# Performance work log

Hardware: AMD Instinct MI355X
Metric: run time of the kernel (lower is better)

Reference implementation:

```python
import jax, jax.numpy as jnp
import numpy as np

N = 100000
E = 1200000
D = 64  # g_dim == h2_dim, heads=1


def setup_inputs() -> dict:
    key = jax.random.key(0)
    ks = jax.random.split(key, 12)
    s = 1.0 / np.sqrt(D)
    node_features = jax.random.normal(ks[0], (N, D), dtype=jnp.float32)
    edge_index = jax.random.randint(ks[1], (2, E), 0, N, dtype=jnp.int64)
    edge_type = jax.random.randint(ks[2], (E,), 0, 4, dtype=jnp.int64)
    Wq = jax.random.uniform(ks[3], (D, D), jnp.float32, -s, s)
    bq = jax.random.uniform(ks[4], (D,), jnp.float32, -s, s)
    Wk = jax.random.uniform(ks[5], (D, D), jnp.float32, -s, s)
    bk = jax.random.uniform(ks[6], (D,), jnp.float32, -s, s)
    Wv = jax.random.uniform(ks[7], (D, D), jnp.float32, -s, s)
    bv = jax.random.uniform(ks[8], (D,), jnp.float32, -s, s)
    Wskip = jax.random.uniform(ks[9], (D, D), jnp.float32, -s, s)
    bskip = jax.random.uniform(ks[10], (D,), jnp.float32, -s, s)
    return dict(node_features=node_features, edge_index=edge_index,
                edge_type=edge_type, Wq=Wq, bq=bq, Wk=Wk, bk=bk,
                Wv=Wv, bv=bv, Wskip=Wskip, bskip=bskip)


def _transformer_conv(x, edge_index, Wq, bq, Wk, bk, Wv, bv, Wskip, bskip):
    src, dst = edge_index[0], edge_index[1]
    q = x @ Wq + bq          # [N, D] queries (for targets)
    k = x @ Wk + bk          # [N, D] keys (for sources)
    v = x @ Wv + bv          # [N, D] values (for sources)
    scale = 1.0 / jnp.sqrt(jnp.asarray(D, x.dtype))
    # per-edge attention logits: (q_dst . k_src) / sqrt(D)   [E]
    logits = jnp.sum(q[dst] * k[src], axis=-1) * scale
    # segment softmax over incoming edges of each destination node
    seg_max = jax.ops.segment_max(logits, dst, num_segments=N)
    seg_max = jnp.where(jnp.isfinite(seg_max), seg_max, 0.0)
    ex = jnp.exp(logits - seg_max[dst])
    seg_sum = jax.ops.segment_sum(ex, dst, num_segments=N)
    alpha = ex / (seg_sum[dst] + 1e-16)                      # [E]
    # attention-weighted scatter-aggregate of source values
    out = jax.ops.segment_sum(alpha[:, None] * v[src], dst, num_segments=N)
    # root/skip connection
    return out + x @ Wskip + bskip


def reference(node_features, edge_index, edge_type, Wq, bq, Wk, bk, Wv, bv, Wskip, bskip):
    # edge_type is accepted but unused, matching the original forward.
    return _transformer_conv(node_features, edge_index, Wq, bq, Wk, bk, Wv, bv, Wskip, bskip)
```

## Files before the change

kernel.cpp:

```cpp
#include <hip/hip_runtime.h>
#include <hip/hip_fp16.h>

#define D 64
#define BSH 9
#define SPLIT_CH 1024
#define NH 512
#define QSCALE 0.18033688f

typedef _Float16 f16x2 __attribute__((ext_vector_type(2)));
typedef _Float16 f16x8 __attribute__((ext_vector_type(8)));
typedef float f32x4 __attribute__((ext_vector_type(4)));

__device__ __forceinline__ float fdot2f(f16x2 a, f16x2 b, float c) {
#if __has_builtin(__builtin_amdgcn_fdot2)
    return __builtin_amdgcn_fdot2(a, b, c, false);
#else
    return fmaf((float)a.x, (float)b.x, fmaf((float)a.y, (float)b.y, c));
#endif
}

__device__ __forceinline__ f16x2 shxor_h2(f16x2 v, int m) {
    int i = __builtin_bit_cast(int, v);
    i = __shfl_xor(i, m);
    return __builtin_bit_cast(f16x2, i);
}

__device__ __forceinline__ unsigned packh2(float a, float b) {
    __half2 h = __floats2half2_rn(a, b);
    return __builtin_bit_cast(unsigned, h);
}

__global__ __launch_bounds__(256) void k_prep(
    const float* __restrict__ Wq, const float* __restrict__ Wk,
    const float* __restrict__ Wv, const float* __restrict__ Wsk,
    const float* __restrict__ bq, const float* __restrict__ bk,
    const float* __restrict__ bv, const float* __restrict__ bsk,
    const int* __restrict__ ei, unsigned* __restrict__ wpk,
    float* __restrict__ ball, int* __restrict__ ghist, int e_cnt)
{
    const int t = threadIdx.x;
    if (blockIdx.x < 32) {
        const int u    = blockIdx.x * 256 + t;
        const int i2   = u & 3;
        const int lane = (u >> 2) & 63;
        const int ks   = (u >> 8) & 1;
        const int mt   = u >> 9;
        const int ncol = mt * 16 + (lane & 15);
        const int k0   = ks * 32 + ((lane >> 4) << 3) + (i2 << 1);
        const float* W; int c; float sc = 1.f;
        if      (ncol <  64) { W = Wq;  c = ncol;       sc = QSCALE; }
        else if (ncol < 128) { W = Wk;  c = ncol - 64;  }
        else if (ncol < 192) { W = Wv;  c = ncol - 128; }
        else                 { W = Wsk; c = ncol - 192; }
        wpk[u] = packh2(W[k0 * 64 + c] * sc, W[(k0 + 1) * 64 + c] * sc);
    } else if (blockIdx.x == 32) {
        float b;
        if      (t <  64) b = bq[t] * QSCALE;
        else if (t < 128) b = bk[t - 64];
        else if (t < 192) b = bv[t - 128];
        else              b = bsk[t - 192];
        ball[t] = b;
    } else {
        __shared__ int h[256];
        h[t] = 0;
        __syncthreads();
        const int hb    = blockIdx.x - 33;
        const int chunk = (e_cnt + NH - 1) / NH;
        const int c0    = hb * chunk;
        const int c1    = min(c0 + chunk, e_cnt);
        for (int i = c0 + t; i < c1; i += 256)
            atomicAdd(&h[ei[e_cnt + i] >> BSH], 1);
        __syncthreads();
        if (h[t]) atomicAdd(&ghist[t], h[t]);
    }
}

__global__ __launch_bounds__(256) void k_splitlin(
    const float* __restrict__ x, const unsigned* __restrict__ wpk,
    const float* __restrict__ ball, const int* __restrict__ ei,
    const int* __restrict__ ghist, int* __restrict__ gcur0,
    unsigned* __restrict__ qh, unsigned* __restrict__ kvh,
    float* __restrict__ out, unsigned* __restrict__ epack,
    int n, int e_cnt, int NSPLIT)
{
    __shared__ __align__(16) union {
        struct {
            unsigned vals[SPLIT_CH];
            unsigned char bkt[SPLIT_CH];
            int hist[256], start[256], cur[256], base[256], s2[256], sg[256];
        } sp;
        _Float16 xsh[16][72];
    } sm;
    const int t = threadIdx.x;

    if (blockIdx.x < NSPLIT) {
        unsigned* vals = sm.sp.vals;
        unsigned char* bkt = sm.sp.bkt;
        int* hist  = sm.sp.hist;
        int* start = sm.sp.start;
        int* cur   = sm.sp.cur;
        int* base  = sm.sp.base;
        int* s2    = sm.sp.s2;
        int* sg    = sm.sp.sg;

        const int e0  = blockIdx.x * SPLIT_CH;
        const int cnt = min(SPLIT_CH, e_cnt - e0);

        hist[t] = 0;
        __syncthreads();
        for (int i = t; i < cnt; i += 256)
            atomicAdd(&hist[ei[e_cnt + e0 + i] >> BSH], 1);
        __syncthreads();

        {
            const int v = hist[t];
            const int g = ghist[t];
            s2[t] = v;
            sg[t] = g;
            __syncthreads();
            for (int off = 1; off < 256; off <<= 1) {
                const int a1 = (t >= off) ? s2[t - off] : 0;
                const int a2 = (t >= off) ? sg[t - off] : 0;
                __syncthreads();
                s2[t] += a1;
                sg[t] += a2;
                __syncthreads();
            }
            start[t] = s2[t] - v;
            cur[t]   = s2[t] - v;
            base[t]  = v ? (sg[t] - g + atomicAdd(&gcur0[t], v)) : 0;
        }
        __syncthreads();

        for (int i = t; i < cnt; i += 256) {
            const int s = ei[e0 + i];
            const int d = ei[e_cnt + e0 + i];
            const int b = d >> BSH;
            const int r = atomicAdd(&cur[b], 1);
            vals[r] = ((unsigned)s << BSH) | (unsigned)(d & 511);
            bkt[r]  = (unsigned char)b;
        }
        __syncthreads();

        for (int i = t; i < cnt; i += 256) {
            const int b = bkt[i];
            epack[base[b] + (i - start[b])] = vals[i];
        }
        return;
    }

    const int node0 = (blockIdx.x - NSPLIT) * 16;
    {
        const float4* xg = (const float4*)(x + (size_t)node0 * 64);
        const int row = t >> 4, c4 = (t & 15) << 2;
        if (node0 + row < n) {
            const float4 v = xg[t];
            f16x2* dst = (f16x2*)&sm.xsh[row][c4];
            dst[0] = f16x2{(_Float16)v.x, (_Float16)v.y};
            dst[1] = f16x2{(_Float16)v.z, (_Float16)v.w};
        }
    }
    __syncthreads();

    const int w  = t >> 6;
    const int l  = t & 63;
    const int nd = l & 15;
    const int kg = l >> 4;

    f32x4 acc0 = {0.f, 0.f, 0.f, 0.f};
    f32x4 acc1 = acc0, acc2 = acc0, acc3 = acc0;
    const uint4* wpk4 = (const uint4*)wpk;

#pragma unroll
    for (int ks = 0; ks < 2; ++ks) {
        const f16x8 bfrag = *(const f16x8*)&sm.xsh[nd][ks * 32 + kg * 8];
        const int fb = (w * 4 * 2 + ks) * 64 + l;
        const f16x8 a0 = __builtin_bit_cast(f16x8, wpk4[fb]);
        const f16x8 a1 = __builtin_bit_cast(f16x8, wpk4[fb + 128]);
        const f16x8 a2 = __builtin_bit_cast(f16x8, wpk4[fb + 256]);
        const f16x8 a3 = __builtin_bit_cast(f16x8, wpk4[fb + 384]);
        acc0 = __builtin_amdgcn_mfma_f32_16x16x32_f16(a0, bfrag, acc0, 0, 0, 0);
        acc1 = __builtin_amdgcn_mfma_f32_16x16x32_f16(a1, bfrag, acc1, 0, 0, 0);
        acc2 = __builtin_amdgcn_mfma_f32_16x16x32_f16(a2, bfrag, acc2, 0, 0, 0);
        acc3 = __builtin_amdgcn_mfma_f32_16x16x32_f16(a3, bfrag, acc3, 0, 0, 0);
    }

    const int node = node0 + nd;
    if (node >= n) return;

    f32x4 accs[4] = {acc0, acc1, acc2, acc3};
#pragma unroll
    for (int m4 = 0; m4 < 4; ++m4) {
        const int gc = (w * 4 + m4) * 16 + kg * 4;
        const float4 bb = ((const float4*)ball)[gc >> 2];
        const float v0 = accs[m4][0] + bb.x;
        const float v1 = accs[m4][1] + bb.y;
        const float v2 = accs[m4][2] + bb.z;
        const float v3 = accs[m4][3] + bb.w;
        if (w == 3) {
            ((float4*)out)[(size_t)node * 16 + ((gc - 192) >> 2)] =
                make_float4(v0, v1, v2, v3);
        } else {
            uint2 u;
            u.x = packh2(v0, v1);
            u.y = packh2(v2, v3);
            if (w == 0)
                ((uint2*)qh)[(size_t)node * 16 + (gc >> 2)] = u;
            else if (w == 1)
                ((uint2*)kvh)[(size_t)node * 32 + ((gc - 64) >> 2)] = u;
            else
                ((uint2*)kvh)[(size_t)node * 32 + 16 + ((gc - 128) >> 2)] = u;
        }
    }
}

__global__ __launch_bounds__(512) void k_nodesort(
    const unsigned* __restrict__ epack, const int* __restrict__ ghist,
    int* __restrict__ esrc, int* __restrict__ endoff, int n)
{
    __shared__ int h[512], cur[512], s[512];
    __shared__ int sbase;
    const int b = blockIdx.x;
    const int t = threadIdx.x;

    s[t] = (t < 256) ? ghist[t] : 0;
    __syncthreads();
    for (int off = 1; off < 512; off <<= 1) {
        const int add = (t >= off) ? s[t - off] : 0;
        __syncthreads();
        s[t] += add;
        __syncthreads();
    }
    if (t == 0) sbase = (b == 0) ? 0 : s[b - 1];
    __syncthreads();
    const int base = sbase;
    const int cnt  = ghist[b];

    h[t] = 0;
    __syncthreads();
    for (int i = t; i < cnt; i += 512)
        atomicAdd(&h[epack[base + i] & 511], 1);
    __syncthreads();

    const int v = h[t];
    s[t] = v;
    __syncthreads();
    for (int off = 1; off < 512; off <<= 1) {
        const int add = (t >= off) ? s[t - off] : 0;
        __syncthreads();
        s[t] += add;
        __syncthreads();
    }
    cur[t] = s[t] - v;
    const int node = (b << BSH) + t;
    if (node < n) endoff[node] = base + s[t];
    __syncthreads();

    for (int i = t; i < cnt; i += 512) {
        const unsigned p = epack[base + i];
        const int r = atomicAdd(&cur[p & 511], 1);
        esrc[base + r] = (int)(p >> BSH);
    }
}

__global__ __launch_bounds__(256) void k_attn(
    const uint4* __restrict__ qh4, const uint4* __restrict__ kv4,
    const int* __restrict__ endoff, const int* __restrict__ esrc,
    float* __restrict__ out, int n)
{
    const int t = threadIdx.x;
    const int node = blockIdx.x * 4 + (t >> 6);
    if (node >= n) return;
    const int lane = t & 63;
    const int g = lane >> 3;
    const int l = lane & 7;

    const int beg = (node == 0) ? 0 : endoff[node - 1];
    const int end = endoff[node];
    const int last = end - 1;

    float4 o0 = make_float4(0.f, 0.f, 0.f, 0.f);
    float4 o1 = o0;
    if (g == 0) {
        o0 = ((const float4*)out)[(size_t)node * 16 + 2 * l];
        o1 = ((const float4*)out)[(size_t)node * 16 + 2 * l + 1];
    }

    const uint4 qu = qh4[(size_t)node * 8 + l];
    const f16x2* qp = (const f16x2*)&qu;

    f16x2 a0 = {(_Float16)0.f, (_Float16)0.f};
    f16x2 a1 = a0, a2 = a0, a3 = a0;
    float den = 0.f;

    int b2 = beg;
    for (; end - b2 > 8; b2 += 16) {
        const int iA = b2 + 2 * g;
        const int iB = iA + 1;
        const int sA = esrc[min(iA, last)];
        const int sB = esrc[min(iB, last)];
        const uint4 kuA = kv4[(size_t)sA * 16 + l];
        const uint4 vuA = kv4[(size_t)sA * 16 + 8 + l];
        const uint4 kuB = kv4[(size_t)sB * 16 + l];
        const uint4 vuB = kv4[(size_t)sB * 16 + 8 + l];
        const f16x2* kpA = (const f16x2*)&kuA;
        const f16x2* vpA = (const f16x2*)&vuA;
        const f16x2* kpB = (const f16x2*)&kuB;
        const f16x2* vpB = (const f16x2*)&vuB;

        float dA = fdot2f(qp[0], kpA[0], 0.f);
        float dB = fdot2f(qp[0], kpB[0], 0.f);
        dA = fdot2f(qp[1], kpA[1], dA);
        dB = fdot2f(qp[1], kpB[1], dB);
        dA = fdot2f(qp[2], kpA[2], dA);
        dB = fdot2f(qp[2], kpB[2], dB);
        dA = fdot2f(qp[3], kpA[3], dA);
        dB = fdot2f(qp[3], kpB[3], dB);
        dA += __shfl_xor(dA, 1);  dB += __shfl_xor(dB, 1);
        dA += __shfl_xor(dA, 2);  dB += __shfl_xor(dB, 2);
        dA += __shfl_xor(dA, 4);  dB += __shfl_xor(dB, 4);

        const float eA = (iA < end) ? exp2f(dA) : 0.f;
        const float eB = (iB < end) ? exp2f(dB) : 0.f;
        den += eA + eB;
        const _Float16 ehA = (_Float16)eA;
        const _Float16 ehB = (_Float16)eB;
        const f16x2 e2A = {ehA, ehA};
        const f16x2 e2B = {ehB, ehB};
        a0 += e2A * vpA[0];  a0 += e2B * vpB[0];
        a1 += e2A * vpA[1];  a1 += e2B * vpB[1];
        a2 += e2A * vpA[2];  a2 += e2B * vpB[2];
        a3 += e2A * vpA[3];  a3 += e2B * vpB[3];
    }
    for (; b2 < end; b2 += 8) {
        const int i = b2 + g;
        const int s = esrc[min(i, last)];
        const uint4 ku = kv4[(size_t)s * 16 + l];
        const uint4 vu = kv4[(size_t)s * 16 + 8 + l];
        const f16x2* kp = (const f16x2*)&ku;
        const f16x2* vp = (const f16x2*)&vu;

        float d = fdot2f(qp[0], kp[0], 0.f);
        d = fdot2f(qp[1], kp[1], d);
        d = fdot2f(qp[2], kp[2], d);
        d = fdot2f(qp[3], kp[3], d);
        d += __shfl_xor(d, 1);
        d += __shfl_xor(d, 2);
        d += __shfl_xor(d, 4);

        const float e = (i < end) ? exp2f(d) : 0.f;
        den += e;
        const _Float16 eh = (_Float16)e;
        const f16x2 e2 = {eh, eh};
        a0 += e2 * vp[0];
        a1 += e2 * vp[1];
        a2 += e2 * vp[2];
        a3 += e2 * vp[3];
    }

#pragma unroll
    for (int m = 8; m <= 32; m <<= 1) {
        den += __shfl_xor(den, m);
        a0 += shxor_h2(a0, m);
        a1 += shxor_h2(a1, m);
        a2 += shxor_h2(a2, m);
        a3 += shxor_h2(a3, m);
    }

    if (g == 0) {
        const float inv = 1.f / (den + 1e-16f);
        float4 r0, r1;
        r0.x = o0.x + (float)a0.x * inv;
        r0.y = o0.y + (float)a0.y * inv;
        r0.z = o0.z + (float)a1.x * inv;
        r0.w = o0.w + (float)a1.y * inv;
        r1.x = o1.x + (float)a2.x * inv;
        r1.y = o1.y + (float)a2.y * inv;
        r1.z = o1.z + (float)a3.x * inv;
        r1.w = o1.w + (float)a3.y * inv;
        ((float4*)out)[(size_t)node * 16 + 2 * l]     = r0;
        ((float4*)out)[(size_t)node * 16 + 2 * l + 1] = r1;
    }
}

extern "C" void kernel_launch(void* const* d_in, const int* in_sizes, int n_in,
                              void* d_out, int out_size, void* d_ws, size_t ws_size,
                              hipStream_t stream)
{
    const float* x   = (const float*)d_in[0];
    const int*   ei  = (const int*)d_in[1];
    const float* Wq  = (const float*)d_in[3];
    const float* bq  = (const float*)d_in[4];
    const float* Wk  = (const float*)d_in[5];
    const float* bk  = (const float*)d_in[6];
    const float* Wv  = (const float*)d_in[7];
    const float* bv  = (const float*)d_in[8];
    const float* Wsk = (const float*)d_in[9];
    const float* bsk = (const float*)d_in[10];
    float* out = (float*)d_out;

    const int n      = in_sizes[0] / D;
    const int e_cnt  = in_sizes[1] / 2;
    const int nbkt   = (n + 511) >> BSH;
    const int NLIN   = (n + 15) / 16;
    const int NSPLIT = (e_cnt + SPLIT_CH - 1) / SPLIT_CH;

    unsigned* qh     = (unsigned*)d_ws;
    unsigned* kvh    = qh + (size_t)n * 32;
    int*      esrc   = (int*)(kvh + (size_t)n * 64);
    unsigned* epack  = (unsigned*)(esrc + e_cnt);
    int*      endoff = (int*)(epack + e_cnt);
    int*      ghist  = endoff + n;
    int*      gcur0  = ghist + 256;
    float*    ball   = (float*)(gcur0 + 256);
    unsigned* wpk    = (unsigned*)(ball + 256);

    hipMemsetAsync(ghist, 0, 512 * sizeof(int), stream);

    k_prep<<<33 + NH, 256, 0, stream>>>(
        Wq, Wk, Wv, Wsk, bq, bk, bv, bsk, ei, wpk, ball, ghist, e_cnt);

    k_splitlin<<<NSPLIT + NLIN, 256, 0, stream>>>(
        x, wpk, ball, ei, ghist, gcur0, qh, kvh, out, epack, n, e_cnt, NSPLIT);

    k_nodesort<<<nbkt, 512, 0, stream>>>(
        epack, ghist, esrc, endoff, n);

    k_attn<<<(n + 3) / 4, 256, 0, stream>>>(
        (const uint4*)qh, (const uint4*)kvh, endoff, esrc, out, n);
}
```

Before: 134.6 us.

## Fuse all stages into one cooperative persistent kernel with grid syncs

Replaces the four separate launches (prep/histogram, split+linear, node sort, attention) with a single cooperative kernel that uses grid-wide syncs between phases and grid-stride loops over work. The aim is to remove launch gaps and tail effects between kernels. The split chunk size is doubled, and the node-sort phase now runs with 256 threads handling two nodes each. In exchange it adds grid barriers, depends on cooperative launch and occupancy queries on the host, and caps the persistent grid size, which may reduce parallelism in the attention phase.

```diff
diff --git a/kernel.cpp b/kernel.cpp
--- a/kernel.cpp
+++ b/kernel.cpp
@@ -1,10 +1,12 @@
 #include <hip/hip_runtime.h>
 #include <hip/hip_fp16.h>
+#include <hip/hip_cooperative_groups.h>
+
+namespace cg = cooperative_groups;
 
 #define D 64
 #define BSH 9
-#define SPLIT_CH 1024
-#define NH 512
+#define SPLIT_CH 2048
 #define QSCALE 0.18033688f
 
 typedef _Float16 f16x2 __attribute__((ext_vector_type(2)));
@@ -30,17 +32,42 @@
     return __builtin_bit_cast(unsigned, h);
 }
 
-__global__ __launch_bounds__(256) void k_prep(
-    const float* __restrict__ Wq, const float* __restrict__ Wk,
-    const float* __restrict__ Wv, const float* __restrict__ Wsk,
-    const float* __restrict__ bq, const float* __restrict__ bk,
-    const float* __restrict__ bv, const float* __restrict__ bsk,
-    const int* __restrict__ ei, unsigned* __restrict__ wpk,
-    float* __restrict__ ball, int* __restrict__ ghist, int e_cnt)
+union SMem {
+    int hist0[256];
+    struct {
+        unsigned vals[SPLIT_CH];
+        unsigned char bkt[SPLIT_CH];
+        int hist[256], start[256], cur[256], base[256], s2[256], sg[256];
+    } sp;
+    struct { __align__(16) _Float16 xsh[16][72]; } lin;
+    struct { int h[512], ex[512], cur[512], sA[256]; } ns;
+};
+
+__global__ __launch_bounds__(256, 8) void k_mega(
+    const float* __restrict__ x, const int* __restrict__ ei,
+    const float* __restrict__ Wq, const float* __restrict__ bq,
+    const float* __restrict__ Wk, const float* __restrict__ bk,
+    const float* __restrict__ Wv, const float* __restrict__ bv,
+    const float* __restrict__ Wsk, const float* __restrict__ bsk,
+    unsigned* __restrict__ wpk, float* __restrict__ ball,
+    int* __restrict__ ghist, int* __restrict__ gcur0,
+    unsigned* __restrict__ qh, unsigned* __restrict__ kvh,
+    unsigned* __restrict__ epack, int* __restrict__ esrc,
+    int* __restrict__ endoff, float* __restrict__ out,
+    int n, int e_cnt)
 {
-    const int t = threadIdx.x;
-    if (blockIdx.x < 32) {
-        const int u    = blockIdx.x * 256 + t;
+    __shared__ SMem sm;
+    cg::grid_group gg = cg::this_grid();
+    const int nb  = (int)gridDim.x;
+    const int bid = (int)blockIdx.x;
+    const int t   = (int)threadIdx.x;
+
+    const int NLIN   = (n + 15) >> 4;
+    const int NSPLIT = (e_cnt + SPLIT_CH - 1) / SPLIT_CH;
+    const int nbkt   = (n + 511) >> BSH;
+
+    if (bid < 32) {
+        const int u    = bid * 256 + t;
         const int i2   = u & 3;
         const int lane = (u >> 2) & 63;
         const int ks   = (u >> 8) & 1;
@@ -53,333 +80,311 @@
         else if (ncol < 192) { W = Wv;  c = ncol - 128; }
         else                 { W = Wsk; c = ncol - 192; }
         wpk[u] = packh2(W[k0 * 64 + c] * sc, W[(k0 + 1) * 64 + c] * sc);
-    } else if (blockIdx.x == 32) {
+    } else if (bid == 32) {
         float b;
         if      (t <  64) b = bq[t] * QSCALE;
         else if (t < 128) b = bk[t - 64];
         else if (t < 192) b = bv[t - 128];
         else              b = bsk[t - 192];
         ball[t] = b;
-    } else {
-        __shared__ int h[256];
+    }
+    {
+        int* h = sm.hist0;
         h[t] = 0;
         __syncthreads();
-        const int hb    = blockIdx.x - 33;
-        const int chunk = (e_cnt + NH - 1) / NH;
-        const int c0    = hb * chunk;
-        const int c1    = min(c0 + chunk, e_cnt);
-        for (int i = c0 + t; i < c1; i += 256)
+        for (int i = bid * 256 + t; i < e_cnt; i += nb * 256)
             atomicAdd(&h[ei[e_cnt + i] >> BSH], 1);
         __syncthreads();
         if (h[t]) atomicAdd(&ghist[t], h[t]);
     }
-}
-
-__global__ __launch_bounds__(256) void k_splitlin(
-    const float* __restrict__ x, const unsigned* __restrict__ wpk,
-    const float* __restrict__ ball, const int* __restrict__ ei,
-    const int* __restrict__ ghist, int* __restrict__ gcur0,
-    unsigned* __restrict__ qh, unsigned* __restrict__ kvh,
-    float* __restrict__ out, unsigned* __restrict__ epack,
-    int n, int e_cnt, int NSPLIT)
-{
-    __shared__ __align__(16) union {
-        struct {
-            unsigned vals[SPLIT_CH];
-            unsigned char bkt[SPLIT_CH];
-            int hist[256], start[256], cur[256], base[256], s2[256], sg[256];
-        } sp;
-        _Float16 xsh[16][72];
-    } sm;
-    const int t = threadIdx.x;
-
-    if (blockIdx.x < NSPLIT) {
-        unsigned* vals = sm.sp.vals;
-        unsigned char* bkt = sm.sp.bkt;
-        int* hist  = sm.sp.hist;
-        int* start = sm.sp.start;
-        int* cur   = sm.sp.cur;
-        int* base  = sm.sp.base;
-        int* s2    = sm.sp.s2;
-        int* sg    = sm.sp.sg;
-
-        const int e0  = blockIdx.x * SPLIT_CH;
-        const int cnt = min(SPLIT_CH, e_cnt - e0);
-
-        hist[t] = 0;
+    gg.sync();
+
+    const int SP = min(NSPLIT, nb >> 1);
+    if (bid < SP) {
+        for (int cidx = bid; cidx < NSPLIT; cidx += SP) {
+            const int e0  = cidx * SPLIT_CH;
+            const int cnt = min(SPLIT_CH, e_cnt - e0);
+
+            sm.sp.hist[t] = 0;
+            __syncthreads();
+            for (int i = t; i < cnt; i += 256)
+                atomicAdd(&sm.sp.hist[ei[e_cnt + e0 + i] >> BSH], 1);
+            __syncthreads();
+
+            {
+                const int v = sm.sp.hist[t];
+                const int g = ghist[t];
+                sm.sp.s2[t] = v;
+                sm.sp.sg[t] = g;
+                __syncthreads();
+                for (int off = 1; off < 256; off <<= 1) {
+                    const int a1 = (t >= off) ? sm.sp.s2[t - off] : 0;
+                    const int a2 = (t >= off) ? sm.sp.sg[t - off] : 0;
+                    __syncthreads();
+                    sm.sp.s2[t] += a1;
+                    sm.sp.sg[t] += a2;
+                    __syncthreads();
+                }
+                sm.sp.start[t] = sm.sp.s2[t] - v;
+                sm.sp.cur[t]   = sm.sp.s2[t] - v;
+                sm.sp.base[t]  = v ? (sm.sp.sg[t] - g + atomicAdd(&gcur0[t], v)) : 0;
+            }
+            __syncthreads();
+
+            for (int i = t; i < cnt; i += 256) {
+                const int s = ei[e0 + i];
+                const int d = ei[e_cnt + e0 + i];
+                const int b = d >> BSH;
+                const int r = atomicAdd(&sm.sp.cur[b], 1);
+                sm.sp.vals[r] = ((unsigned)s << BSH) | (unsigned)(d & 511);
+                sm.sp.bkt[r]  = (unsigned char)b;
+            }
+            __syncthreads();
+
+            for (int i = t; i < cnt; i += 256) {
+                const int b = sm.sp.bkt[i];
+                epack[sm.sp.base[b] + (i - sm.sp.start[b])] = sm.sp.vals[i];
+            }
+            __syncthreads();
+        }
+    } else {
+        const int lb  = bid - SP;
+        const int nlb = nb - SP;
+        const uint4* wpk4 = (const uint4*)wpk;
+        for (int tile = lb; tile < NLIN; tile += nlb) {
+            const int node0 = tile * 16;
+            {
+                const float4* xg = (const float4*)(x + (size_t)node0 * 64);
+                const int row = t >> 4, c4 = (t & 15) << 2;
+                if (node0 + row < n) {
+                    const float4 v = xg[t];
+                    f16x2* dst = (f16x2*)&sm.lin.xsh[row][c4];
+                    dst[0] = f16x2{(_Float16)v.x, (_Float16)v.y};
+                    dst[1] = f16x2{(_Float16)v.z, (_Float16)v.w};
+                }
+            }
+            __syncthreads();
+
+            const int w  = t >> 6;
+            const int l  = t & 63;
+            const int nd = l & 15;
+            const int kg = l >> 4;
+
+            f32x4 acc0 = {0.f, 0.f, 0.f, 0.f};
+            f32x4 acc1 = acc0, acc2 = acc0, acc3 = acc0;
+#pragma unroll
+            for (int ks = 0; ks < 2; ++ks) {
+                const f16x8 bfrag = *(const f16x8*)&sm.lin.xsh[nd][ks * 32 + kg * 8];
+                const int fb = (w * 4 * 2 + ks) * 64 + l;
+                const f16x8 a0 = __builtin_bit_cast(f16x8, wpk4[fb]);
+                const f16x8 a1 = __builtin_bit_cast(f16x8, wpk4[fb + 128]);
+                const f16x8 a2 = __builtin_bit_cast(f16x8, wpk4[fb + 256]);
+                const f16x8 a3 = __builtin_bit_cast(f16x8, wpk4[fb + 384]);
+                acc0 = __builtin_amdgcn_mfma_f32_16x16x32_f16(a0, bfrag, acc0, 0, 0, 0);
+                acc1 = __builtin_amdgcn_mfma_f32_16x16x32_f16(a1, bfrag, acc1, 0, 0, 0);
+                acc2 = __builtin_amdgcn_mfma_f32_16x16x32_f16(a2, bfrag, acc2, 0, 0, 0);
+                acc3 = __builtin_amdgcn_mfma_f32_16x16x32_f16(a3, bfrag, acc3, 0, 0, 0);
+            }
+
+            const int node = node0 + nd;
+            if (node < n) {
+                f32x4 accs[4] = {acc0, acc1, acc2, acc3};
+#pragma unroll
+                for (int m4 = 0; m4 < 4; ++m4) {
+                    const int gc = (w * 4 + m4) * 16 + kg * 4;
+                    const float4 bb = ((const float4*)ball)[gc >> 2];
+                    const float v0 = accs[m4][0] + bb.x;
+                    const float v1 = accs[m4][1] + bb.y;
+                    const float v2 = accs[m4][2] + bb.z;
+                    const float v3 = accs[m4][3] + bb.w;
+                    if (w == 3) {
+                        ((float4*)out)[(size_t)node * 16 + ((gc - 192) >> 2)] =
+                            make_float4(v0, v1, v2, v3);
+                    } else {
+                        uint2 u;
+                        u.x = packh2(v0, v1);
+                        u.y = packh2(v2, v3);
+                        if (w == 0)
+                            ((uint2*)qh)[(size_t)node * 16 + (gc >> 2)] = u;
+                        else if (w == 1)
+                            ((uint2*)kvh)[(size_t)node * 32 + ((gc - 64) >> 2)] = u;
+                        else
+                            ((uint2*)kvh)[(size_t)node * 32 + 16 + ((gc - 128) >> 2)] = u;
+                    }
+                }
+            }
+            __syncthreads();
+        }
+    }
+    gg.sync();
+
+    if (bid < nbkt) {
+        int* h   = sm.ns.h;
+        int* ex  = sm.ns.ex;
+        int* cur = sm.ns.cur;
+        int* sA  = sm.ns.sA;
+
+        sA[t] = ghist[t];
+        __syncthreads();
+        for (int off = 1; off < 256; off <<= 1) {
+            const int add = (t >= off) ? sA[t - off] : 0;
+            __syncthreads();
+            sA[t] += add;
+            __syncthreads();
+        }
+        const int base = (bid == 0) ? 0 : sA[bid - 1];
+        const int cnt  = ghist[bid];
+
+        h[t] = 0; h[t + 256] = 0;
         __syncthreads();
         for (int i = t; i < cnt; i += 256)
-            atomicAdd(&hist[ei[e_cnt + e0 + i] >> BSH], 1);
-        __syncthreads();
-
-        {
-            const int v = hist[t];
-            const int g = ghist[t];
-            s2[t] = v;
-            sg[t] = g;
-            __syncthreads();
-            for (int off = 1; off < 256; off <<= 1) {
-                const int a1 = (t >= off) ? s2[t - off] : 0;
-                const int a2 = (t >= off) ? sg[t - off] : 0;
-                __syncthreads();
-                s2[t] += a1;
-                sg[t] += a2;
-                __syncthreads();
-            }
-            start[t] = s2[t] - v;
-            cur[t]   = s2[t] - v;
-            base[t]  = v ? (sg[t] - g + atomicAdd(&gcur0[t], v)) : 0;
-        }
+            atomicAdd(&h[epack[base + i] & 511], 1);
+        __syncthreads();
+
+        const int p0 = h[2 * t], p1 = h[2 * t + 1];
+        sA[t] = p0 + p1;
+        __syncthreads();
+        for (int off = 1; off < 256; off <<= 1) {
+            const int add = (t >= off) ? sA[t - off] : 0;
+            __syncthreads();
+            sA[t] += add;
+            __syncthreads();
+        }
+        const int exc = sA[t] - (p0 + p1);
+        ex[2 * t]     = exc;
+        ex[2 * t + 1] = exc + p0;
+        cur[2 * t]     = exc;
+        cur[2 * t + 1] = exc + p0;
+        const int node0 = (bid << BSH) + 2 * t;
+        if (node0     < n) endoff[node0]     = base + exc + p0;
+        if (node0 + 1 < n) endoff[node0 + 1] = base + exc + p0 + p1;
         __syncthreads();
 
         for (int i = t; i < cnt; i += 256) {
-            const int s = ei[e0 + i];
-            const int d = ei[e_cnt + e0 + i];
-            const int b = d >> BSH;
-            const int r = atomicAdd(&cur[b], 1);
-            vals[r] = ((unsigned)s << BSH) | (unsigned)(d & 511);
-            bkt[r]  = (unsigned char)b;
-        }
-        __syncthreads();
-
-        for (int i = t; i < cnt; i += 256) {
-            const int b = bkt[i];
-            epack[base[b] + (i - start[b])] = vals[i];
-        }
-        return;
+            const unsigned p = epack[base + i];
+            const int r = atomicAdd(&cur[p & 511], 1);
+            esrc[base + r] = (int)(p >> BSH);
+        }
     }
-
-    const int node0 = (blockIdx.x - NSPLIT) * 16;
-    {
-        const float4* xg = (const float4*)(x + (size_t)node0 * 64);
-        const int row = t >> 4, c4 = (t & 15) << 2;
-        if (node0 + row < n) {
-            const float4 v = xg[t];
-            f16x2* dst = (f16x2*)&sm.xsh[row][c4];
-            dst[0] = f16x2{(_Float16)v.x, (_Float16)v.y};
-            dst[1] = f16x2{(_Float16)v.z, (_Float16)v.w};
-        }
-    }
-    __syncthreads();
-
-    const int w  = t >> 6;
-    const int l  = t & 63;
-    const int nd = l & 15;
-    const int kg = l >> 4;
-
-    f32x4 acc0 = {0.f, 0.f, 0.f, 0.f};
-    f32x4 acc1 = acc0, acc2 = acc0, acc3 = acc0;
-    const uint4* wpk4 = (const uint4*)wpk;
+    gg.sync();
+
+    const int nq = (n + 3) >> 2;
+    const uint4* qh4 = (const uint4*)qh;
+    const uint4* kv4 = (const uint4*)kvh;
+    for (int qd = bid; qd < nq; qd += nb) {
+        const int node = qd * 4 + (t >> 6);
+        if (node < n) {
+            const int lane = t & 63;
+            const int g = lane >> 3;
+            const int l = lane & 7;
+
+            const int beg = (node == 0) ? 0 : endoff[node - 1];
+            const int end = endoff[node];
+            const int last = end - 1;
+
+            float4 o0 = make_float4(0.f, 0.f, 0.f, 0.f);
+            float4 o1 = o0;
+            if (g == 0) {
+                o0 = ((const float4*)out)[(size_t)node * 16 + 2 * l];
+                o1 = ((const float4*)out)[(size_t)node * 16 + 2 * l + 1];
+            }
+
+            const uint4 qu = qh4[(size_t)node * 8 + l];
+            const f16x2* qp = (const f16x2*)&qu;
+
+            f16x2 a0 = {(_Float16)0.f, (_Float16)0.f};
+            f16x2 a1 = a0, a2 = a0, a3 = a0;
+            float den = 0.f;
+
+            int b2 = beg;
+            for (; end - b2 > 8; b2 += 16) {
+                const int iA = b2 + 2 * g;
+                const int iB = iA + 1;
+                const int sA_ = esrc[min(iA, last)];
+                const int sB_ = esrc[min(iB, last)];
+                const uint4 kuA = kv4[(size_t)sA_ * 16 + l];
+                const uint4 vuA = kv4[(size_t)sA_ * 16 + 8 + l];
+                const uint4 kuB = kv4[(size_t)sB_ * 16 + l];
+                const uint4 vuB = kv4[(size_t)sB_ * 16 + 8 + l];
+                const f16x2* kpA = (const f16x2*)&kuA;
+                const f16x2* vpA = (const f16x2*)&vuA;
+                const f16x2* kpB = (const f16x2*)&kuB;
+                const f16x2* vpB = (const f16x2*)&vuB;
+
+                float dA = fdot2f(qp[0], kpA[0], 0.f);
+                float dB = fdot2f(qp[0], kpB[0], 0.f);
+                dA = fdot2f(qp[1], kpA[1], dA);
+                dB = fdot2f(qp[1], kpB[1], dB);
+                dA = fdot2f(qp[2], kpA[2], dA);
+                dB = fdot2f(qp[2], kpB[2], dB);
+                dA = fdot2f(qp[3], kpA[3], dA);
+                dB = fdot2f(qp[3], kpB[3], dB);
+                dA += __shfl_xor(dA, 1);  dB += __shfl_xor(dB, 1);
+                dA += __shfl_xor(dA, 2);  dB += __shfl_xor(dB, 2);
+                dA += __shfl_xor(dA, 4);  dB += __shfl_xor(dB, 4);
+
+                const float eA = (iA < end) ? exp2f(dA) : 0.f;
+                const float eB = (iB < end) ? exp2f(dB) : 0.f;
+                den += eA + eB;
+                const _Float16 ehA = (_Float16)eA;
+                const _Float16 ehB = (_Float16)eB;
+                const f16x2 e2A = {ehA, ehA};
+                const f16x2 e2B = {ehB, ehB};
+                a0 += e2A * vpA[0];  a0 += e2B * vpB[0];
+                a1 += e2A * vpA[1];  a1 += e2B * vpB[1];
+                a2 += e2A * vpA[2];  a2 += e2B * vpB[2];
+                a3 += e2A * vpA[3];  a3 += e2B * vpB[3];
+            }
+            for (; b2 < end; b2 += 8) {
+                const int i = b2 + g;
+                const int s = esrc[min(i, last)];
+                const uint4 ku = kv4[(size_t)s * 16 + l];
+                const uint4 vu = kv4[(size_t)s * 16 + 8 + l];
+                const f16x2* kp = (const f16x2*)&ku;
+                const f16x2* vp = (const f16x2*)&vu;
+
+                float d = fdot2f(qp[0], kp[0], 0.f);
+                d = fdot2f(qp[1], kp[1], d);
+                d = fdot2f(qp[2], kp[2], d);
+                d = fdot2f(qp[3], kp[3], d);
+                d += __shfl_xor(d, 1);
+                d += __shfl_xor(d, 2);
+                d += __shfl_xor(d, 4);
+
+                const float e = (i < end) ? exp2f(d) : 0.f;
+                den += e;
+                const _Float16 eh = (_Float16)e;
+                const f16x2 e2 = {eh, eh};
+                a0 += e2 * vp[0];
+                a1 += e2 * vp[1];
+                a2 += e2 * vp[2];
+                a3 += e2 * vp[3];
+            }
 
 #pragma unroll
-    for (int ks = 0; ks < 2; ++ks) {
-        const f16x8 bfrag = *(const f16x8*)&sm.xsh[nd][ks * 32 + kg * 8];
-        const int fb = (w * 4 * 2 + ks) * 64 + l;
-        const f16x8 a0 = __builtin_bit_cast(f16x8, wpk4[fb]);
-        const f16x8 a1 = __builtin_bit_cast(f16x8, wpk4[fb + 128]);
-        const f16x8 a2 = __builtin_bit_cast(f16x8, wpk4[fb + 256]);
-        const f16x8 a3 = __builtin_bit_cast(f16x8, wpk4[fb + 384]);
-        acc0 = __builtin_amdgcn_mfma_f32_16x16x32_f16(a0, bfrag, acc0, 0, 0, 0);
-        acc1 = __builtin_amdgcn_mfma_f32_16x16x32_f16(a1, bfrag, acc1, 0, 0, 0);
-        acc2 = __builtin_amdgcn_mfma_f32_16x16x32_f16(a2, bfrag, acc2, 0, 0, 0);
-        acc3 = __builtin_amdgcn_mfma_f32_16x16x32_f16(a3, bfrag, acc3, 0, 0, 0);
-    }
-
-    const int node = node0 + nd;
-    if (node >= n) return;
-
-    f32x4 accs[4] = {acc0, acc1, acc2, acc3};
-#pragma unroll
-    for (int m4 = 0; m4 < 4; ++m4) {
-        const int gc = (w * 4 + m4) * 16 + kg * 4;
-        const float4 bb = ((const float4*)ball)[gc >> 2];
-        const float v0 = accs[m4][0] + bb.x;
-        const float v1 = accs[m4][1] + bb.y;
-        const float v2 = accs[m4][2] + bb.z;
-        const float v3 = accs[m4][3] + bb.w;
-        if (w == 3) {
-            ((float4*)out)[(size_t)node * 16 + ((gc - 192) >> 2)] =
-                make_float4(v0, v1, v2, v3);
-        } else {
-            uint2 u;
-            u.x = packh2(v0, v1);
-            u.y = packh2(v2, v3);
-            if (w == 0)
-                ((uint2*)qh)[(size_t)node * 16 + (gc >> 2)] = u;
-            else if (w == 1)
-                ((uint2*)kvh)[(size_t)node * 32 + ((gc - 64) >> 2)] = u;
-            else
-                ((uint2*)kvh)[(size_t)node * 32 + 16 + ((gc - 128) >> 2)] = u;
-        }
-    }
-}
-
-__global__ __launch_bounds__(512) void k_nodesort(
-    const unsigned* __restrict__ epack, const int* __restrict__ ghist,
-    int* __restrict__ esrc, int* __restrict__ endoff, int n)
-{
-    __shared__ int h[512], cur[512], s[512];
-    __shared__ int sbase;
-    const int b = blockIdx.x;
-    const int t = threadIdx.x;
-
-    s[t] = (t < 256) ? ghist[t] : 0;
-    __syncthreads();
-    for (int off = 1; off < 512; off <<= 1) {
-        const int add = (t >= off) ? s[t - off] : 0;
-        __syncthreads();
-        s[t] += add;
-        __syncthreads();
-    }
-    if (t == 0) sbase = (b == 0) ? 0 : s[b - 1];
-    __syncthreads();
-    const int base = sbase;
-    const int cnt  = ghist[b];
-
-    h[t] = 0;
-    __syncthreads();
-    for (int i = t; i < cnt; i += 512)
-        atomicAdd(&h[epack[base + i] & 511], 1);
-    __syncthreads();
-
-    const int v = h[t];
-    s[t] = v;
-    __syncthreads();
-    for (int off = 1; off < 512; off <<= 1) {
-        const int add = (t >= off) ? s[t - off] : 0;
-        __syncthreads();
-        s[t] += add;
-        __syncthreads();
-    }
-    cur[t] = s[t] - v;
-    const int node = (b << BSH) + t;
-    if (node < n) endoff[node] = base + s[t];
-    __syncthreads();
-
-    for (int i = t; i < cnt; i += 512) {
-        const unsigned p = epack[base + i];
-        const int r = atomicAdd(&cur[p & 511], 1);
-        esrc[base + r] = (int)(p >> BSH);
-    }
-}
-
-__global__ __launch_bounds__(256) void k_attn(
-    const uint4* __restrict__ qh4, const uint4* __restrict__ kv4,
-    const int* __restrict__ endoff, const int* __restrict__ esrc,
-    float* __restrict__ out, int n)
-{
-    const int t = threadIdx.x;
-    const int node = blockIdx.x * 4 + (t >> 6);
-    if (node >= n) return;
-    const int lane = t & 63;
-    const int g = lane >> 3;
-    const int l = lane & 7;
-
-    const int beg = (node == 0) ? 0 : endoff[node - 1];
-    const int end = endoff[node];
-    const int last = end - 1;
-
-    float4 o0 = make_float4(0.f, 0.f, 0.f, 0.f);
-    float4 o1 = o0;
-    if (g == 0) {
-        o0 = ((const float4*)out)[(size_t)node * 16 + 2 * l];
-        o1 = ((const float4*)out)[(size_t)node * 16 + 2 * l + 1];
-    }
-
-    const uint4 qu = qh4[(size_t)node * 8 + l];
-    const f16x2* qp = (const f16x2*)&qu;
-
-    f16x2 a0 = {(_Float16)0.f, (_Float16)0.f};
-    f16x2 a1 = a0, a2 = a0, a3 = a0;
-    float den = 0.f;
-
-    int b2 = beg;
-    for (; end - b2 > 8; b2 += 16) {
-        const int iA = b2 + 2 * g;
-        const int iB = iA + 1;
-        const int sA = esrc[min(iA, last)];
-        const int sB = esrc[min(iB, last)];
-        const uint4 kuA = kv4[(size_t)sA * 16 + l];
-        const uint4 vuA = kv4[(size_t)sA * 16 + 8 + l];
-        const uint4 kuB = kv4[(size_t)sB * 16 + l];
-        const uint4 vuB = kv4[(size_t)sB * 16 + 8 + l];
-        const f16x2* kpA = (const f16x2*)&kuA;
-        const f16x2* vpA = (const f16x2*)&vuA;
-        const f16x2* kpB = (const f16x2*)&kuB;
-        const f16x2* vpB = (const f16x2*)&vuB;
-
-        float dA = fdot2f(qp[0], kpA[0], 0.f);
-        float dB = fdot2f(qp[0], kpB[0], 0.f);
-        dA = fdot2f(qp[1], kpA[1], dA);
-        dB = fdot2f(qp[1], kpB[1], dB);
-        dA = fdot2f(qp[2], kpA[2], dA);
-        dB = fdot2f(qp[2], kpB[2], dB);
-        dA = fdot2f(qp[3], kpA[3], dA);
-        dB = fdot2f(qp[3], kpB[3], dB);
-        dA += __shfl_xor(dA, 1);  dB += __shfl_xor(dB, 1);
-        dA += __shfl_xor(dA, 2);  dB += __shfl_xor(dB, 2);
-        dA += __shfl_xor(dA, 4);  dB += __shfl_xor(dB, 4);
-
-        const float eA = (iA < end) ? exp2f(dA) : 0.f;
-        const float eB = (iB < end) ? exp2f(dB) : 0.f;
-        den += eA + eB;
-        const _Float16 ehA = (_Float16)eA;
-        const _Float16 ehB = (_Float16)eB;
-        const f16x2 e2A = {ehA, ehA};
-        const f16x2 e2B = {ehB, ehB};
-        a0 += e2A * vpA[0];  a0 += e2B * vpB[0];
-        a1 += e2A * vpA[1];  a1 += e2B * vpB[1];
-        a2 += e2A * vpA[2];  a2 += e2B * vpB[2];
-        a3 += e2A * vpA[3];  a3 += e2B * vpB[3];
-    }
-    for (; b2 < end; b2 += 8) {
-        const int i = b2 + g;
-        const int s = esrc[min(i, last)];
-        const uint4 ku = kv4[(size_t)s * 16 + l];
-        const uint4 vu = kv4[(size_t)s * 16 + 8 + l];
-        const f16x2* kp = (const f16x2*)&ku;
-        const f16x2* vp = (const f16x2*)&vu;
-
-        float d = fdot2f(qp[0], kp[0], 0.f);
-        d = fdot2f(qp[1], kp[1], d);
-        d = fdot2f(qp[2], kp[2], d);
-        d = fdot2f(qp[3], kp[3], d);
-        d += __shfl_xor(d, 1);
-        d += __shfl_xor(d, 2);
-        d += __shfl_xor(d, 4);
-
-        const float e = (i < end) ? exp2f(d) : 0.f;
-        den += e;
-        const _Float16 eh = (_Float16)e;
-        const f16x2 e2 = {eh, eh};
-        a0 += e2 * vp[0];
-        a1 += e2 * vp[1];
-        a2 += e2 * vp[2];
-        a3 += e2 * vp[3];
-    }
-
-#pragma unroll
-    for (int m = 8; m <= 32; m <<= 1) {
-        den += __shfl_xor(den, m);
-        a0 += shxor_h2(a0, m);
-        a1 += shxor_h2(a1, m);
-        a2 += shxor_h2(a2, m);
-        a3 += shxor_h2(a3, m);
-    }
-
-    if (g == 0) {
-        const float inv = 1.f / (den + 1e-16f);
-        float4 r0, r1;
-        r0.x = o0.x + (float)a0.x * inv;
-        r0.y = o0.y + (float)a0.y * inv;
-        r0.z = o0.z + (float)a1.x * inv;
-        r0.w = o0.w + (float)a1.y * inv;
-        r1.x = o1.x + (float)a2.x * inv;
-        r1.y = o1.y + (float)a2.y * inv;
-        r1.z = o1.z + (float)a3.x * inv;
-        r1.w = o1.w + (float)a3.y * inv;
-        ((float4*)out)[(size_t)node * 16 + 2 * l]     = r0;
-        ((float4*)out)[(size_t)node * 16 + 2 * l + 1] = r1;
+            for (int m = 8; m <= 32; m <<= 1) {
+                den += __shfl_xor(den, m);
+                a0 += shxor_h2(a0, m);
+                a1 += shxor_h2(a1, m);
+                a2 += shxor_h2(a2, m);
+                a3 += shxor_h2(a3, m);
+            }
+
+            if (g == 0) {
+                const float inv = 1.f / (den + 1e-16f);
+                float4 r0, r1;
+                r0.x = o0.x + (float)a0.x * inv;
+                r0.y = o0.y + (float)a0.y * inv;
+                r0.z = o0.z + (float)a1.x * inv;
+                r0.w = o0.w + (float)a1.y * inv;
+                r1.x = o1.x + (float)a2.x * inv;
+                r1.y = o1.y + (float)a2.y * inv;
+                r1.z = o1.z + (float)a3.x * inv;
+                r1.w = o1.w + (float)a3.y * inv;
+                ((float4*)out)[(size_t)node * 16 + 2 * l]     = r0;
+                ((float4*)out)[(size_t)node * 16 + 2 * l + 1] = r1;
+            }
+        }
     }
 }
 
@@ -399,11 +404,8 @@
     const float* bsk = (const float*)d_in[10];
     float* out = (float*)d_out;
 
-    const int n      = in_sizes[0] / D;
-    const int e_cnt  = in_sizes[1] / 2;
-    const int nbkt   = (n + 511) >> BSH;
-    const int NLIN   = (n + 15) / 16;
-    const int NSPLIT = (e_cnt + SPLIT_CH - 1) / SPLIT_CH;
+    int n     = in_sizes[0] / D;
+    int e_cnt = in_sizes[1] / 2;
 
     unsigned* qh     = (unsigned*)d_ws;
     unsigned* kvh    = qh + (size_t)n * 32;
@@ -417,15 +419,20 @@
 
     hipMemsetAsync(ghist, 0, 512 * sizeof(int), stream);
 
-    k_prep<<<33 + NH, 256, 0, stream>>>(
-        Wq, Wk, Wv, Wsk, bq, bk, bv, bsk, ei, wpk, ball, ghist, e_cnt);
-
-    k_splitlin<<<NSPLIT + NLIN, 256, 0, stream>>>(
-        x, wpk, ball, ei, ghist, gcur0, qh, kvh, out, epack, n, e_cnt, NSPLIT);
-
-    k_nodesort<<<nbkt, 512, 0, stream>>>(
-        epack, ghist, esrc, endoff, n);
-
-    k_attn<<<(n + 3) / 4, 256, 0, stream>>>(
-        (const uint4*)qh, (const uint4*)kvh, endoff, esrc, out, n);
+    int mpc = 0;
+    hipOccupancyMaxActiveBlocksPerMultiprocessor(&mpc, k_mega, 256, 0);
+    if (mpc < 1) mpc = 1;
+    int grid = mpc * 256;
+    if (grid > 2048) grid = 2048;
+
+    void* args[] = {
+        (void*)&x, (void*)&ei,
+        (void*)&Wq, (void*)&bq, (void*)&Wk, (void*)&bk,
+        (void*)&Wv, (void*)&bv, (void*)&Wsk, (void*)&bsk,
+        (void*)&wpk, (void*)&ball, (void*)&ghist, (void*)&gcur0,
+        (void*)&qh, (void*)&kvh, (void*)&epack, (void*)&esrc,
+        (void*)&endoff, (void*)&out, (void*)&n, (void*)&e_cnt
+    };
+    hipLaunchCooperativeKernel((const void*)k_mega, dim3(grid), dim3(256),
+                               args, 0, stream);
 }
```

Measured after the change: 454.4 us. +237.7%, slower.
